# Kernel tuning notes

Measured on AMD Instinct MI355X. Metric: run time of the kernel, lower is better.

## Reference

```python
import jax, jax.numpy as jnp
import numpy as np
import math

EMBED = 1024
HEADS = 16
HEAD_DIM = EMBED // HEADS
B, S = 2, 2048


def setup_inputs() -> dict:
    key = jax.random.key(0)
    ks = jax.random.split(key, 11)
    s = 1.0 / math.sqrt(EMBED)
    return {
        "query": jax.random.normal(ks[0], (B, S, EMBED), jnp.float32),
        "key_": jax.random.normal(ks[1], (B, S, EMBED), jnp.float32),
        "value": jax.random.normal(ks[2], (B, S, EMBED), jnp.float32),
        "Wq": jax.random.normal(ks[3], (EMBED, EMBED), jnp.float32) * s,
        "bq": jax.random.normal(ks[4], (EMBED,), jnp.float32) * s,
        "Wk": jax.random.normal(ks[5], (EMBED, EMBED), jnp.float32) * s,
        "bk": jax.random.normal(ks[6], (EMBED,), jnp.float32) * s,
        "Wv": jax.random.normal(ks[7], (EMBED, EMBED), jnp.float32) * s,
        "bv": jax.random.normal(ks[8], (EMBED,), jnp.float32) * s,
        "Wo": jax.random.normal(ks[9], (EMBED, EMBED), jnp.float32) * s,
        "bo": jax.random.normal(ks[10], (EMBED,), jnp.float32) * s,
    }


def reference(query, key_, value, Wq, bq, Wk, bk, Wv, bv, Wo, bo):
    b, s, e = query.shape
    # projections (torch Linear: x @ W.T + b)
    q = query @ Wq.T + bq
    k = key_ @ Wk.T + bk
    v = value @ Wv.T + bv
    # [B, H, S, hd]
    q = q.reshape(b, s, HEADS, HEAD_DIM).transpose(0, 2, 1, 3)
    k = k.reshape(b, s, HEADS, HEAD_DIM).transpose(0, 2, 1, 3)
    v = v.reshape(b, s, HEADS, HEAD_DIM).transpose(0, 2, 1, 3)
    scores = jnp.einsum("bhqd,bhkd->bhqk", q, k) / math.sqrt(HEAD_DIM)
    attn = jax.nn.softmax(scores, axis=-1)
    out = jnp.einsum("bhqk,bhkd->bhqd", attn, v)
    out = out.transpose(0, 2, 1, 3).reshape(b, s, e)
    return out @ Wo.T + bo
```

## Files before the change

kernel.cpp:

```cpp
#include <hip/hip_runtime.h>
#include <hip/hip_bf16.h>

using bf16_t = __bf16;
using bf16x2 = __attribute__((ext_vector_type(2))) __bf16;
using bf16x4 = __attribute__((ext_vector_type(4))) __bf16;
using bf16x8 = __attribute__((ext_vector_type(8))) __bf16;
using f32x4  = __attribute__((ext_vector_type(4))) float;
using u32 = unsigned int;
using u32x4 = __attribute__((ext_vector_type(4))) u32;
using i32x2 = __attribute__((ext_vector_type(2))) int;

constexpr int S_ = 2048, E_ = 1024, M_ = 4096;
constexpr size_t MAT_A = (size_t)M_ * E_;
constexpr size_t MAT_W = (size_t)E_ * E_;

__device__ __forceinline__ bf16_t tobf(float f) {
  unsigned u = __builtin_bit_cast(unsigned, f);
  unsigned short r = (unsigned short)((u + 0x7fffu + ((u >> 16) & 1u)) >> 16);
  return __builtin_bit_cast(bf16_t, r);
}
__device__ __forceinline__ u32 packbf2(float a, float b) {
  u32 ua = __builtin_bit_cast(u32, a) + 0x8000u;
  u32 ub = __builtin_bit_cast(u32, b) + 0x8000u;
  return (ua >> 16) | (ub & 0xffff0000u);
}
__device__ __forceinline__ u32 cvtpk(float lo, float hi) {
  bf16x2 t;
  t[0] = (bf16_t)lo;
  t[1] = (bf16_t)hi;
  return __builtin_bit_cast(u32, t);
}
__device__ __forceinline__ void swap32(u32& a, u32& b) {
  i32x2 r = __builtin_amdgcn_permlane32_swap((int)a, (int)b, false, false);
  a = (u32)r[0];
  b = (u32)r[1];
}
__device__ __forceinline__ void swap16(u32& a, u32& b) {
  i32x2 r = __builtin_amdgcn_permlane16_swap((int)a, (int)b, false, false);
  a = (u32)r[0];
  b = (u32)r[1];
}
__device__ __forceinline__ void async_lds16(const bf16_t* g, bf16_t* l) {
  __builtin_amdgcn_global_load_lds(
      (const __attribute__((address_space(1))) unsigned int*)g,
      (__attribute__((address_space(3))) unsigned int*)l, 16, 0, 0);
}

__global__ __launch_bounds__(256) void cvt_all(
    const float* __restrict__ s0, const float* __restrict__ s1,
    const float* __restrict__ s2, const float* __restrict__ s3,
    const float* __restrict__ s4, const float* __restrict__ s5,
    const float* __restrict__ s6,
    bf16_t* __restrict__ d0, bf16_t* __restrict__ d1,
    bf16_t* __restrict__ d2, bf16_t* __restrict__ d3,
    bf16_t* __restrict__ d4, bf16_t* __restrict__ d5,
    bf16_t* __restrict__ d6) {
  size_t i8 = ((size_t)blockIdx.x * 256 + threadIdx.x) * 8;
  const float* s;
  bf16_t* d;
  size_t off;
  if (i8 < 3 * MAT_A) {
    int w = (int)(i8 >> 22);
    off = i8 & (MAT_A - 1);
    s = w == 0 ? s0 : w == 1 ? s1 : s2;
    d = w == 0 ? d0 : w == 1 ? d1 : d2;
  } else {
    size_t j = i8 - 3 * MAT_A;
    int w = (int)(j >> 20);
    off = j & (MAT_W - 1);
    s = w == 0 ? s3 : w == 1 ? s4 : w == 2 ? s5 : s6;
    d = w == 0 ? d3 : w == 1 ? d4 : w == 2 ? d5 : d6;
  }
  float4 a = *(const float4*)(s + off);
  float4 b = *(const float4*)(s + off + 4);
  bf16x8 o;
  o[0] = tobf(a.x); o[1] = tobf(a.y); o[2] = tobf(a.z); o[3] = tobf(a.w);
  o[4] = tobf(b.x); o[5] = tobf(b.y); o[6] = tobf(b.z); o[7] = tobf(b.w);
  *(bf16x8*)(d + off) = o;
}

__global__ __launch_bounds__(256) void gemm_qkv(
    const bf16_t* __restrict__ xq, const bf16_t* __restrict__ xk,
    const bf16_t* __restrict__ xv, const bf16_t* __restrict__ wq,
    const bf16_t* __restrict__ wk, const bf16_t* __restrict__ wv,
    const float* __restrict__ bq, const float* __restrict__ bk,
    const float* __restrict__ bv, bf16_t* __restrict__ outb,
    bf16_t* __restrict__ Vt) {
  constexpr int K = 1024, N = 1024, BK = 64;
  constexpr float SC = 0.18033688011f;
  __shared__ __align__(16) bf16_t smem[18432];
  bf16_t* As = smem;
  bf16_t* Bs = smem + 128 * BK;

  const int which = blockIdx.y >> 3;
  const bf16_t* X = which == 0 ? xq : which == 1 ? xk : xv;
  const bf16_t* W = which == 0 ? wq : which == 1 ? wk : wv;
  const float* bias = which == 0 ? bq : which == 1 ? bk : bv;
  const int row0 = blockIdx.x * 128, col0 = (blockIdx.y & 7) * 128;

  const int tid = threadIdx.x, lane = tid & 63, wave = tid >> 6;
  const int l15 = lane & 15, q = lane >> 4;
  const int wm = (wave & 1) * 64, wn = (wave >> 1) * 64;
  const f32x4 fzero = {0.f, 0.f, 0.f, 0.f};

  f32x4 acc[4][4];
#pragma unroll
  for (int i = 0; i < 4; ++i)
#pragma unroll
    for (int j = 0; j < 4; ++j) acc[i][j] = fzero;

  const int srow = lane >> 3;
  const int schunk = ((lane & 7) ^ srow) * 8;
  const bf16_t* gA = X + (size_t)(row0 + wave * 32 + srow) * K + schunk;
  const bf16_t* gB = W + (size_t)(col0 + wave * 32 + srow) * K + schunk;
  bf16_t* lA = As + wave * 32 * BK;
  bf16_t* lB = Bs + wave * 32 * BK;

  int ck[2];
  ck[0] = ((q) ^ (l15 & 7)) * 8;
  ck[1] = ((4 + q) ^ (l15 & 7)) * 8;

  for (int k0 = 0; k0 < K; k0 += BK) {
    __syncthreads();
#pragma unroll
    for (int p = 0; p < 4; ++p) {
      async_lds16(gA + k0 + (size_t)(p * 8) * K, lA + p * 8 * BK);
      async_lds16(gB + k0 + (size_t)(p * 8) * K, lB + p * 8 * BK);
    }
    __syncthreads();
#pragma unroll
    for (int h = 0; h < 2; ++h) {
      bf16x8 af[4], bw[4];
#pragma unroll
      for (int i = 0; i < 4; ++i)
        af[i] = *(const bf16x8*)(As + (wm + i * 16 + l15) * BK + ck[h]);
#pragma unroll
      for (int j = 0; j < 4; ++j)
        bw[j] = *(const bf16x8*)(Bs + (wn + j * 16 + l15) * BK + ck[h]);
#pragma unroll
      for (int i = 0; i < 4; ++i)
#pragma unroll
        for (int j = 0; j < 4; ++j)
          acc[i][j] = __builtin_amdgcn_mfma_f32_16x16x32_bf16(af[i], bw[j],
                                                              acc[i][j], 0, 0, 0);
    }
  }

  if (which < 2) {
    const float sc = which == 0 ? SC : 1.0f;
    bf16_t* C = outb + (size_t)which * MAT_A;
#pragma unroll
    for (int j = 0; j < 4; ++j) {
      const int col = col0 + wn + j * 16 + l15;
      const float bc = bias[col];
#pragma unroll
      for (int i = 0; i < 4; ++i)
#pragma unroll
        for (int r = 0; r < 4; ++r) {
          const int row = row0 + wm + i * 16 + q * 4 + r;
          C[(size_t)row * N + col] = tobf((acc[i][j][r] + bc) * sc);
        }
    }
  } else {
    __syncthreads();
    bf16_t* Ep = smem + wave * 4608;
#pragma unroll
    for (int j = 0; j < 4; ++j) {
      const float bc = bias[col0 + wn + j * 16 + l15];
      const int nl = j * 16 + l15;
#pragma unroll
      for (int i = 0; i < 4; ++i) {
        uint2 pk;
        pk.x = packbf2(acc[i][j][0] + bc, acc[i][j][1] + bc);
        pk.y = packbf2(acc[i][j][2] + bc, acc[i][j][3] + bc);
        *(uint2*)(Ep + nl * 72 + i * 16 + q * 4) = pk;
      }
    }
    const int head = (col0 + wn) >> 6;
    const int tok0 = row0 + wm;
    const int bb = tok0 >> 11, tokb = tok0 & 2047;
    const int dl = lane >> 3, ml = (lane & 7) * 8;
#pragma unroll
    for (int p = 0; p < 8; ++p) {
      const int d = dl + p * 8;
      bf16x8 v = *(const bf16x8*)(Ep + d * 72 + ml);
      *(bf16x8*)(Vt + ((size_t)((bb * 16 + head) * 64 + d)) * S_ + tokb + ml) = v;
    }
  }
}

__global__ __launch_bounds__(256) void gemm_o(const bf16_t* __restrict__ X,
                                              const bf16_t* __restrict__ W,
                                              const float* __restrict__ bias,
                                              float* __restrict__ C) {
  constexpr int K = 1024, N = 1024, BK = 64;
  __shared__ __align__(16) bf16_t As[64 * BK];
  __shared__ __align__(16) bf16_t Bs[128 * BK];
  const int tid = threadIdx.x, lane = tid & 63, wave = tid >> 6;
  const int l15 = lane & 15, q = lane >> 4;
  const int row0 = blockIdx.x * 64, col0 = blockIdx.y * 128;
  const int wm = (wave & 1) * 32, wn = (wave >> 1) * 64;
  const f32x4 fzero = {0.f, 0.f, 0.f, 0.f};

  f32x4 acc[2][4];
#pragma unroll
  for (int i = 0; i < 2; ++i)
#pragma unroll
    for (int j = 0; j < 4; ++j) acc[i][j] = fzero;

  const int srow = lane >> 3;
  const int schunk = ((lane & 7) ^ srow) * 8;
  const bf16_t* gA = X + (size_t)(row0 + wave * 16 + srow) * K + schunk;
  const bf16_t* gB = W + (size_t)(col0 + wave * 32 + srow) * K + schunk;
  bf16_t* lA = As + wave * 16 * BK;
  bf16_t* lB = Bs + wave * 32 * BK;

  int ck[2];
  ck[0] = ((q) ^ (l15 & 7)) * 8;
  ck[1] = ((4 + q) ^ (l15 & 7)) * 8;

  for (int k0 = 0; k0 < K; k0 += BK) {
    __syncthreads();
    async_lds16(gA + k0, lA);
    async_lds16(gA + k0 + (size_t)8 * K, lA + 8 * BK);
#pragma unroll
    for (int p = 0; p < 4; ++p)
      async_lds16(gB + k0 + (size_t)(p * 8) * K, lB + p * 8 * BK);
    __syncthreads();
#pragma unroll
    for (int h = 0; h < 2; ++h) {
      bf16x8 af[2], bw[4];
#pragma unroll
      for (int i = 0; i < 2; ++i)
        af[i] = *(const bf16x8*)(As + (wm + i * 16 + l15) * BK + ck[h]);
#pragma unroll
      for (int j = 0; j < 4; ++j)
        bw[j] = *(const bf16x8*)(Bs + (wn + j * 16 + l15) * BK + ck[h]);
#pragma unroll
      for (int i = 0; i < 2; ++i)
#pragma unroll
        for (int j = 0; j < 4; ++j)
          acc[i][j] = __builtin_amdgcn_mfma_f32_16x16x32_bf16(af[i], bw[j],
                                                              acc[i][j], 0, 0, 0);
    }
  }

#pragma unroll
  for (int j = 0; j < 4; ++j) {
    const int col = col0 + wn + j * 16 + l15;
    const float bc = bias[col];
#pragma unroll
    for (int i = 0; i < 2; ++i)
#pragma unroll
      for (int r = 0; r < 4; ++r) {
        const int row = row0 + wm + i * 16 + q * 4 + r;
        C[(size_t)row * N + col] = acc[i][j][r] + bc;
      }
  }
}

__global__ __launch_bounds__(256, 2) void attn_mfma(
    const bf16_t* __restrict__ Qm, const bf16_t* __restrict__ Km,
    const bf16_t* __restrict__ Vtg, bf16_t* __restrict__ Om) {
  __shared__ __align__(16) bf16_t Ks[2][64 * 64];
  __shared__ __align__(16) bf16_t Vs[2][64 * 64];

  const int tid = threadIdx.x, lane = tid & 63, wave = tid >> 6;
  const int l15 = lane & 15, q = lane >> 4;
  const int bh = blockIdx.x & 31, qb = blockIdx.x >> 5;
  const int b = bh >> 4, h = bh & 15;
  const size_t rowbase = (size_t)b * S_;
  const int hcol = h * 64;
  const int q0 = qb * 128 + wave * 32;

  const int srow = lane >> 3;
  const int schunk = (lane & 7) ^ srow;
  const bf16_t* gK = Km + (rowbase + wave * 16 + srow) * E_ + hcol + schunk * 8;
  const bf16_t* gV = Vtg + ((size_t)bh * 64 + wave * 16 + srow) * S_ + schunk * 8;

  bf16x8 qf[2][2];
#pragma unroll
  for (int qt = 0; qt < 2; ++qt) {
    const bf16_t* qp = Qm + (rowbase + q0 + qt * 16 + l15) * E_ + hcol + q * 8;
    qf[qt][0] = *(const bf16x8*)qp;
    qf[qt][1] = *(const bf16x8*)(qp + 32);
  }

  bf16x8 onesv;
#pragma unroll
  for (int j = 0; j < 8; ++j)
    onesv[j] = __builtin_bit_cast(bf16_t, (unsigned short)0x3F80);

  const f32x4 fzero = {0.f, 0.f, 0.f, 0.f};
  f32x4 oacc[2][4];
#pragma unroll
  for (int qt = 0; qt < 2; ++qt)
#pragma unroll
    for (int mt = 0; mt < 4; ++mt) oacc[qt][mt] = fzero;
  f32x4 lsacc[2] = {fzero, fzero};

  const int rbase = l15 * 64;
  int ck[2];
  ck[0] = ((q) ^ (l15 & 7)) * 8;
  ck[1] = ((4 + q) ^ (l15 & 7)) * 8;

  async_lds16(gK, Ks[0] + wave * 1024);
  async_lds16(gK + (size_t)8 * E_, Ks[0] + wave * 1024 + 512);
  async_lds16(gV, Vs[0] + wave * 1024);
  async_lds16(gV + (size_t)8 * S_, Vs[0] + wave * 1024 + 512);

  for (int t = 0; t < 32; ++t) {
    const int pb = t & 1;
    __syncthreads();
    if (t + 1 < 32) {
      const size_t koff = (size_t)((t + 1) * 64) * E_;
      const int voff = (t + 1) * 64;
      bf16_t* dK = Ks[pb ^ 1] + wave * 1024;
      bf16_t* dV = Vs[pb ^ 1] + wave * 1024;
      async_lds16(gK + koff, dK);
      async_lds16(gK + koff + (size_t)8 * E_, dK + 512);
      async_lds16(gV + voff, dV);
      async_lds16(gV + voff + (size_t)8 * S_, dV + 512);
    }
    const bf16_t* Kbuf = Ks[pb];
    const bf16_t* Vbuf = Vs[pb];

    u32 uu[2][4][2];
#pragma unroll
    for (int nt = 0; nt < 4; ++nt) {
      bf16x8 a0 = *(const bf16x8*)(Kbuf + nt * 1024 + rbase + ck[0]);
      bf16x8 a1 = *(const bf16x8*)(Kbuf + nt * 1024 + rbase + ck[1]);
#pragma unroll
      for (int qt = 0; qt < 2; ++qt) {
        f32x4 st = fzero;
        st = __builtin_amdgcn_mfma_f32_16x16x32_bf16(a0, qf[qt][0], st, 0, 0, 0);
        st = __builtin_amdgcn_mfma_f32_16x16x32_bf16(a1, qf[qt][1], st, 0, 0, 0);
        uu[qt][nt][0] =
            cvtpk(__builtin_amdgcn_exp2f(st[0]), __builtin_amdgcn_exp2f(st[1]));
        uu[qt][nt][1] =
            cvtpk(__builtin_amdgcn_exp2f(st[2]), __builtin_amdgcn_exp2f(st[3]));
      }
    }

#pragma unroll
    for (int kk = 0; kk < 2; ++kk) {
      bf16x8 bp[2];
#pragma unroll
      for (int qt = 0; qt < 2; ++qt) {
        u32 A = uu[qt][2 * kk][0], Bv = uu[qt][2 * kk][1];
        u32 C = uu[qt][2 * kk + 1][0], D = uu[qt][2 * kk + 1][1];
        swap32(A, C);  swap16(A, C);
        swap32(Bv, D); swap16(Bv, D);
        u32x4 w = {A, Bv, C, D};
        bp[qt] = __builtin_bit_cast(bf16x8, w);
        lsacc[qt] =
            __builtin_amdgcn_mfma_f32_16x16x32_bf16(onesv, bp[qt], lsacc[qt], 0, 0, 0);
      }
      __builtin_amdgcn_s_setprio(1);
#pragma unroll
      for (int mt = 0; mt < 4; ++mt) {
        bf16x8 av = *(const bf16x8*)(Vbuf + mt * 1024 + rbase + ck[kk]);
        oacc[0][mt] =
            __builtin_amdgcn_mfma_f32_16x16x32_bf16(av, bp[0], oacc[0][mt], 0, 0, 0);
        oacc[1][mt] =
            __builtin_amdgcn_mfma_f32_16x16x32_bf16(av, bp[1], oacc[1][mt], 0, 0, 0);
      }
      __builtin_amdgcn_s_setprio(0);
    }
  }

#pragma unroll
  for (int qt = 0; qt < 2; ++qt) {
    const float inv = 1.0f / lsacc[qt][0];
    const size_t orow = (rowbase + q0 + qt * 16 + l15) * E_ + hcol + q * 4;
#pragma unroll
    for (int mt = 0; mt < 4; ++mt) {
      bf16x4 o;
#pragma unroll
      for (int r = 0; r < 4; ++r) o[r] = tobf(oacc[qt][mt][r] * inv);
      *(bf16x4*)(Om + orow + mt * 16) = o;
    }
  }
}

extern "C" void kernel_launch(void* const* d_in, const int* in_sizes, int n_in,
                              void* d_out, int out_size, void* d_ws, size_t ws_size,
                              hipStream_t stream) {
  const float* query = (const float*)d_in[0];
  const float* key_  = (const float*)d_in[1];
  const float* value = (const float*)d_in[2];
  const float* Wq = (const float*)d_in[3];
  const float* bq = (const float*)d_in[4];
  const float* Wk = (const float*)d_in[5];
  const float* bk = (const float*)d_in[6];
  const float* Wv = (const float*)d_in[7];
  const float* bv = (const float*)d_in[8];
  const float* Wo = (const float*)d_in[9];
  const float* bo = (const float*)d_in[10];

  bf16_t* qc  = (bf16_t*)d_ws;
  bf16_t* kc  = qc + MAT_A;
  bf16_t* vc  = kc + MAT_A;
  bf16_t* wqb = vc + MAT_A;
  bf16_t* wkb = wqb + MAT_W;
  bf16_t* wvb = wkb + MAT_W;
  bf16_t* wob = wvb + MAT_W;
  bf16_t* Qb  = wob + MAT_W;
  bf16_t* Kb  = Qb + MAT_A;
  bf16_t* Vt  = Kb + MAT_A;
  bf16_t* AOb = Vt + MAT_A;

  cvt_all<<<8192, 256, 0, stream>>>(query, key_, value, Wq, Wk, Wv, Wo,
                                    qc, kc, vc, wqb, wkb, wvb, wob);
  gemm_qkv<<<dim3(32, 24), 256, 0, stream>>>(qc, kc, vc, wqb, wkb, wvb,
                                             bq, bk, bv, Qb, Vt);
  attn_mfma<<<512, 256, 0, stream>>>(Qb, Kb, Vt, AOb);
  gemm_o<<<dim3(64, 8), 256, 0, stream>>>(AOb, wob, bo, (float*)d_out);
}
```

Before: 210.8 us.

## Double-buffer LDS tiles in QKV and output projection GEMMs

Both projection GEMMs now hold two LDS stages. The next K-tile is fetched asynchronously while MFMAs run on the current one, and one of the two barriers per iteration is removed. The aim is to hide global-to-LDS latency behind compute. The trade-off is more LDS per block: the QKV GEMM grows from 36KB to 64KB, which may reduce occupancy. Correctness also depends on the async loads being complete at the single remaining barrier.

```diff
diff --git a/kernel.cpp b/kernel.cpp
--- a/kernel.cpp
+++ b/kernel.cpp
@@ -88,9 +88,7 @@
     bf16_t* __restrict__ Vt) {
   constexpr int K = 1024, N = 1024, BK = 64;
   constexpr float SC = 0.18033688011f;
-  __shared__ __align__(16) bf16_t smem[18432];
-  bf16_t* As = smem;
-  bf16_t* Bs = smem + 128 * BK;
+  __shared__ __align__(16) bf16_t smem[2][16384];
 
   const int which = blockIdx.y >> 3;
   const bf16_t* X = which == 0 ? xq : which == 1 ? xk : xv;
@@ -113,21 +111,33 @@
   const int schunk = ((lane & 7) ^ srow) * 8;
   const bf16_t* gA = X + (size_t)(row0 + wave * 32 + srow) * K + schunk;
   const bf16_t* gB = W + (size_t)(col0 + wave * 32 + srow) * K + schunk;
-  bf16_t* lA = As + wave * 32 * BK;
-  bf16_t* lB = Bs + wave * 32 * BK;
+  const int lofs = wave * 32 * BK;
 
   int ck[2];
   ck[0] = ((q) ^ (l15 & 7)) * 8;
   ck[1] = ((4 + q) ^ (l15 & 7)) * 8;
 
-  for (int k0 = 0; k0 < K; k0 += BK) {
+#pragma unroll
+  for (int p = 0; p < 4; ++p) {
+    async_lds16(gA + (size_t)(p * 8) * K, smem[0] + lofs + p * 8 * BK);
+    async_lds16(gB + (size_t)(p * 8) * K, smem[0] + 8192 + lofs + p * 8 * BK);
+  }
+
+  for (int it = 0; it < 16; ++it) {
+    const int cur = it & 1;
     __syncthreads();
-#pragma unroll
-    for (int p = 0; p < 4; ++p) {
-      async_lds16(gA + k0 + (size_t)(p * 8) * K, lA + p * 8 * BK);
-      async_lds16(gB + k0 + (size_t)(p * 8) * K, lB + p * 8 * BK);
-    }
-    __syncthreads();
+    if (it + 1 < 16) {
+      const int k1 = (it + 1) * BK;
+      bf16_t* dA = smem[cur ^ 1] + lofs;
+      bf16_t* dB = smem[cur ^ 1] + 8192 + lofs;
+#pragma unroll
+      for (int p = 0; p < 4; ++p) {
+        async_lds16(gA + k1 + (size_t)(p * 8) * K, dA + p * 8 * BK);
+        async_lds16(gB + k1 + (size_t)(p * 8) * K, dB + p * 8 * BK);
+      }
+    }
+    const bf16_t* As = smem[cur];
+    const bf16_t* Bs = smem[cur] + 8192;
 #pragma unroll
     for (int h = 0; h < 2; ++h) {
       bf16x8 af[4], bw[4];
@@ -163,7 +173,7 @@
     }
   } else {
     __syncthreads();
-    bf16_t* Ep = smem + wave * 4608;
+    bf16_t* Ep = &smem[0][0] + wave * 4608;
 #pragma unroll
     for (int j = 0; j < 4; ++j) {
       const float bc = bias[col0 + wn + j * 16 + l15];
@@ -194,8 +204,7 @@
                                               const float* __restrict__ bias,
                                               float* __restrict__ C) {
   constexpr int K = 1024, N = 1024, BK = 64;
-  __shared__ __align__(16) bf16_t As[64 * BK];
-  __shared__ __align__(16) bf16_t Bs[128 * BK];
+  __shared__ __align__(16) bf16_t smem[2][12288];
   const int tid = threadIdx.x, lane = tid & 63, wave = tid >> 6;
   const int l15 = lane & 15, q = lane >> 4;
   const int row0 = blockIdx.x * 64, col0 = blockIdx.y * 128;
@@ -212,21 +221,34 @@
   const int schunk = ((lane & 7) ^ srow) * 8;
   const bf16_t* gA = X + (size_t)(row0 + wave * 16 + srow) * K + schunk;
   const bf16_t* gB = W + (size_t)(col0 + wave * 32 + srow) * K + schunk;
-  bf16_t* lA = As + wave * 16 * BK;
-  bf16_t* lB = Bs + wave * 32 * BK;
+  const int lofsA = wave * 16 * BK;
+  const int lofsB = wave * 32 * BK;
 
   int ck[2];
   ck[0] = ((q) ^ (l15 & 7)) * 8;
   ck[1] = ((4 + q) ^ (l15 & 7)) * 8;
 
-  for (int k0 = 0; k0 < K; k0 += BK) {
+  async_lds16(gA, smem[0] + lofsA);
+  async_lds16(gA + (size_t)8 * K, smem[0] + lofsA + 8 * BK);
+#pragma unroll
+  for (int p = 0; p < 4; ++p)
+    async_lds16(gB + (size_t)(p * 8) * K, smem[0] + 4096 + lofsB + p * 8 * BK);
+
+  for (int it = 0; it < 16; ++it) {
+    const int cur = it & 1;
     __syncthreads();
-    async_lds16(gA + k0, lA);
-    async_lds16(gA + k0 + (size_t)8 * K, lA + 8 * BK);
-#pragma unroll
-    for (int p = 0; p < 4; ++p)
-      async_lds16(gB + k0 + (size_t)(p * 8) * K, lB + p * 8 * BK);
-    __syncthreads();
+    if (it + 1 < 16) {
+      const int k1 = (it + 1) * BK;
+      bf16_t* dA = smem[cur ^ 1] + lofsA;
+      bf16_t* dB = smem[cur ^ 1] + 4096 + lofsB;
+      async_lds16(gA + k1, dA);
+      async_lds16(gA + k1 + (size_t)8 * K, dA + 8 * BK);
+#pragma unroll
+      for (int p = 0; p < 4; ++p)
+        async_lds16(gB + k1 + (size_t)(p * 8) * K, dB + p * 8 * BK);
+    }
+    const bf16_t* As = smem[cur];
+    const bf16_t* Bs = smem[cur] + 4096;
 #pragma unroll
     for (int h = 0; h < 2; ++h) {
       bf16x8 af[2], bw[4];
```

Measured after the change: 208.4 us. About the same (-1.1%).
